# Kernel optimization log

Measured on AMD Instinct MI355X. Metric: run time of the kernel, lower is better.

## Reference

```python
import jax, jax.numpy as jnp
import numpy as np

N_ITER = 3
B, L, U = 32, 120, 640
INPUT_CAPS = 32 * 9 * 12  # 3456
N_CLASSES = 5
FINAL_DIM = 16
N_REL = 25


def squash(x):
    # x: (B, n_caps, dim); squash along dim (axis=2)
    l2 = jnp.sum(x * x, axis=2, keepdims=True)
    return x * (l2 / (1.0 + l2) / jnp.sqrt(l2))


def conv2d(x, w, b, stride):
    out = jax.lax.conv_general_dilated(
        x, w, window_strides=stride, padding='VALID',
        dimension_numbers=('NCHW', 'OIHW', 'NCHW'))
    return out + b[None, :, None, None]


def setup_inputs() -> dict:
    key = jax.random.key(0)
    ks = jax.random.split(key, 10)
    stdv = 1.0 / np.sqrt(INPUT_CAPS)
    return {
        'input': jax.random.normal(ks[0], (B, 1, L, U), jnp.float32),
        'conv1_w': jax.random.normal(ks[1], (256, 1, L // 4, U // 4), jnp.float32) * 0.02,
        'conv1_b': jnp.zeros((256,), jnp.float32),
        'prim_w': jax.random.normal(ks[2], (256, 256, 10, 10), jnp.float32) * 0.02,
        'prim_b': jnp.zeros((256,), jnp.float32),
        'caps_w': jax.random.uniform(ks[3], (INPUT_CAPS, 8, N_CLASSES * FINAL_DIM),
                                     jnp.float32, -stdv, stdv),
        'b_route': jnp.zeros((INPUT_CAPS, N_CLASSES), jnp.float32),
        'pred_w': jax.random.normal(ks[4], (N_REL, FINAL_DIM), jnp.float32) * 0.1,
        'pred_b': jnp.zeros((N_REL,), jnp.float32),
        'eos_w': jax.random.normal(ks[5], (1, FINAL_DIM), jnp.float32) * 0.1,
        'eos_b': jnp.zeros((1,), jnp.float32),
    }


def reference(input, conv1_w, conv1_b, prim_w, prim_b, caps_w, b_route,
              pred_w, pred_b, eos_w, eos_b):
    # conv1 + relu: (B,1,120,640) -> (B,256,91,121)
    x = jax.nn.relu(conv2d(input, conv1_w, conv1_b, (1, 4)))
    # primary caps conv: -> (B,256,9,12)
    out = conv2d(x, prim_w, prim_b, (10, 10))
    n, _, h, w = out.shape
    out = out.reshape(n, 32, 8, h, w)                 # (B,32,8,9,12)
    out = jnp.transpose(out, (0, 1, 3, 4, 2))         # (B,32,9,12,8)
    u = squash(out.reshape(n, -1, 8))                 # (B,3456,8)
    # caps layer prediction: (B,I,8) x (I,8,O*D) -> (B,I,O,D)
    u_predict = jnp.einsum('bic,icj->bij', u, caps_w)
    u_predict = u_predict.reshape(n, INPUT_CAPS, N_CLASSES, FINAL_DIM)
    # agreement routing
    c = jax.nn.softmax(b_route, axis=1)               # (I,O)
    s = jnp.einsum('io,biod->bod', c, u_predict)
    v = squash(s)
    b_batch = jnp.broadcast_to(b_route, (n, INPUT_CAPS, N_CLASSES))
    for _ in range(N_ITER):
        b_batch = b_batch + jnp.einsum('biod,bod->bio', u_predict, v)
        c = jax.nn.softmax(b_batch, axis=-1)          # (B,I,O)
        s = jnp.einsum('bio,biod->bod', c, u_predict)
        v = squash(s)                                 # (B,O,D)
    predict_logits = v @ pred_w.T + pred_b            # (B,O,25)
    eos_logits = v @ eos_w.T + eos_b                  # (B,O,1)
    logits = jnp.concatenate([predict_logits, eos_logits], axis=-1)
    return jax.nn.log_softmax(logits, axis=-1)
```

## Files before the change

kernel.cpp:

```cpp
#include <hip/hip_runtime.h>

typedef __bf16 bf16x8 __attribute__((ext_vector_type(8)));
typedef __bf16 bf16x4 __attribute__((ext_vector_type(4)));
typedef float  f32x4  __attribute__((ext_vector_type(4)));
typedef unsigned int  uint;
typedef unsigned short ushort_t;

static __device__ __forceinline__ ushort_t f2bf(float f) {
    uint u = __float_as_uint(f);
    return (ushort_t)((u + 0x7fffu + ((u >> 16) & 1u)) >> 16);
}
static __device__ __forceinline__ float bf2f(ushort_t u) {
    return __uint_as_float((uint)u << 16);
}
static __device__ __forceinline__ f32x4 up4(uint2 p) {
    f32x4 r;
    r[0] = __uint_as_float(p.x << 16);
    r[1] = __uint_as_float(p.x & 0xffff0000u);
    r[2] = __uint_as_float(p.y << 16);
    r[3] = __uint_as_float(p.y & 0xffff0000u);
    return r;
}


constexpr size_t OFF_W1F = 0;
constexpr size_t SZ_W1F  = (size_t)256 * 4800 * 2;
constexpr size_t OFF_A2  = OFF_W1F + SZ_W1F;
constexpr size_t SZ_A2   = (size_t)256 * 25600 * 2;
constexpr size_t OFF_X   = OFF_A2 + SZ_A2;
constexpr size_t SZ_X    = (size_t)32 * 90 * 120 * 256 * 2;
constexpr size_t OFF_P   = OFF_X + SZ_X;
constexpr size_t SZ_P    = (size_t)8 * 256 * 32 * 112 * 2;
constexpr size_t OFF_UP  = OFF_X;
constexpr size_t OFF_BB  = OFF_X + (size_t)24 * 1024 * 1024;
constexpr size_t OFF_S0  = OFF_X + (size_t)28 * 1024 * 1024;
constexpr size_t OFF_S1  = OFF_X + (size_t)29 * 1024 * 1024;
constexpr size_t WS_NEED = OFF_P + SZ_P;

__global__ void k0_w1(const float* __restrict__ w, ushort_t* __restrict__ o) {
    int t = blockIdx.x * 256 + threadIdx.x;
    int l   = t & 63;
    int q   = t >> 6;
    int kwc = q % 5;
    int ocb = (q / 5) % 16;
    int kh  = q / 80;
    const float* src = w + (size_t)(ocb * 16 + (l & 15)) * 4800 + kh * 160 + kwc * 32 + (l >> 4) * 8;
    float4 f0 = *(const float4*)src;
    float4 f1 = *(const float4*)(src + 4);
    uint4 pk;
    pk.x = (uint)f2bf(f0.x) | ((uint)f2bf(f0.y) << 16);
    pk.y = (uint)f2bf(f0.z) | ((uint)f2bf(f0.w) << 16);
    pk.z = (uint)f2bf(f1.x) | ((uint)f2bf(f1.y) << 16);
    pk.w = (uint)f2bf(f1.z) | ((uint)f2bf(f1.w) << 16);
    *(uint4*)&o[(size_t)t * 8] = pk;
}

__global__ void k0_a2(const float* __restrict__ w, ushort_t* __restrict__ o) {
    __shared__ ushort_t l[25600];
    int oc2 = blockIdx.x;
    const float* src = w + (size_t)oc2 * 25600;
    for (int idx = threadIdx.x; idx < 25600; idx += 256) l[idx] = f2bf(src[idx]);
    __syncthreads();
    ushort_t* dst = o + (size_t)oc2 * 25600;
    for (int idx = threadIdx.x; idx < 25600; idx += 256) {
        int p = idx >> 8, ic = idx & 255;
        dst[idx] = l[ic * 100 + p];
    }
}

__global__ __launch_bounds__(256, 2) void k1_conv1(const float* __restrict__ inp,
                                                   const ushort_t* __restrict__ w1f,
                                                   const float* __restrict__ cb,
                                                   ushort_t* __restrict__ X) {
    __shared__ ushort_t smem[31680];
    ushort_t* brow = smem;
    const int tid = threadIdx.x, lane = tid & 63, wid = tid >> 6;
    const int wm = wid * 64;
    const int h = blockIdx.x, b = blockIdx.y;
    const int l16 = lane & 15, g8 = (lane >> 4) * 8;
    const int bbase = 4 * l16 + g8;
    f32x4 acc[4][8] = {};

    for (int idx = tid; idx < 5280; idx += 256) {
        int r = idx / 176, c = idx % 176;
        uint2 pk; pk.x = 0u; pk.y = 0u;
        if (c < 160) {
            const float* irow = inp + ((size_t)b * 120 + h + r) * 640;
            float4 f = *(const float4*)&irow[c * 4];
            pk.x = (uint)f2bf(f.x) | ((uint)f2bf(f.y) << 16);
            pk.y = (uint)f2bf(f.z) | ((uint)f2bf(f.w) << 16);
        }
        *(uint2*)&brow[r * 704 + c * 4] = pk;
    }
    __syncthreads();

#pragma unroll 1
    for (int kh = 0; kh < 30; ++kh) {
        bf16x8 bc[19];
        const int rb = kh * 704 + bbase;
#pragma unroll
        for (int t = 0; t < 19; ++t) {
            union { bf16x8 v8; bf16x4 v4[2]; } fr;
            fr.v4[0] = *(const bf16x4*)&brow[rb + 32 * t];
            fr.v4[1] = *(const bf16x4*)&brow[rb + 32 * t + 4];
            bc[t] = fr.v8;
        }
#pragma unroll
        for (int kwc = 0; kwc < 5; ++kwc) {
            bf16x8 af[4];
#pragma unroll
            for (int mt = 0; mt < 4; ++mt) {
                int q = (kh * 16 + wid * 4 + mt) * 5 + kwc;
                af[mt] = *(const bf16x8*)&w1f[(size_t)q * 512 + lane * 8];
            }
#pragma unroll
            for (int nt = 0; nt < 8; ++nt)
#pragma unroll
                for (int mt = 0; mt < 4; ++mt)
                    acc[mt][nt] = __builtin_amdgcn_mfma_f32_16x16x32_bf16(af[mt], bc[2 * nt + kwc], acc[mt][nt], 0, 0, 0);
        }
    }

    float cbv[4][4];
#pragma unroll
    for (int mt = 0; mt < 4; ++mt)
#pragma unroll
        for (int r = 0; r < 4; ++r)
            cbv[mt][r] = cb[wm + mt * 16 + (lane >> 4) * 4 + r];
    __syncthreads();
    ushort_t* cs = smem;
#pragma unroll
    for (int nt = 0; nt < 8; ++nt) {
        int wg = nt * 16 + l16;
        if (wg < 120) {
#pragma unroll
            for (int mt = 0; mt < 4; ++mt)
#pragma unroll
                for (int r = 0; r < 4; ++r) {
                    int oc = wm + mt * 16 + (lane >> 4) * 4 + r;
                    float v = acc[mt][nt][r] + cbv[mt][r];
                    v = v > 0.f ? v : 0.f;
                    cs[wg * 264 + oc] = f2bf(v);
                }
        }
    }
    __syncthreads();
    ushort_t* Xbase = X + ((size_t)b * 90 + h) * 120 * 256;
    for (int idx = tid; idx < 3840; idx += 256) {
        int w = idx >> 5, c = (idx & 31) * 8;
        *(uint4*)&Xbase[(size_t)w * 256 + c] = *(const uint4*)&cs[w * 264 + c];
    }
}

__global__ __launch_bounds__(256) void k2_prim(const ushort_t* __restrict__ X,
                                               const ushort_t* __restrict__ A2,
                                               ushort_t* __restrict__ P) {
    const int tid = threadIdx.x, lane = tid & 63, wid = tid >> 6;
    const int mi = blockIdx.x, s = blockIdx.y, b = blockIdx.z;
    const int msub = mi * 128 + wid * 32;
    const int l16 = lane & 15, g8 = (lane >> 4) * 8;
    f32x4 acc[2][7] = {};
    size_t aoff[2];
#pragma unroll
    for (int t = 0; t < 2; ++t) aoff[t] = (size_t)(msub + t * 16 + l16) * 25600 + g8;
    size_t noff[7];
#pragma unroll
    for (int nt = 0; nt < 7; ++nt) {
        int n = nt * 16 + l16; n = n < 108 ? n : 107;
        int h2 = n / 12, w2 = n % 12;
        noff[nt] = (((size_t)b * 90 + 10 * h2) * 120 + 10 * w2) * 256 + g8;
    }
    const int p0 = (100 * s) / 8, p1 = (100 * (s + 1)) / 8;
#pragma unroll 1
    for (int p = p0; p < p1; ++p) {
        int ph = p / 10, pw = p % 10;
        size_t xb = (size_t)(ph * 120 + pw) * 256;
        size_t ab = (size_t)p * 256;
#pragma unroll
        for (int icc = 0; icc < 8; ++icc) {
            bf16x8 af[2], bfr[7];
#pragma unroll
            for (int t = 0; t < 2; ++t)
                af[t] = *(const bf16x8*)&A2[aoff[t] + ab + icc * 32];
#pragma unroll
            for (int nt = 0; nt < 7; ++nt)
                bfr[nt] = *(const bf16x8*)&X[noff[nt] + xb + icc * 32];
#pragma unroll
            for (int t = 0; t < 2; ++t)
#pragma unroll
                for (int nt = 0; nt < 7; ++nt)
                    acc[t][nt] = __builtin_amdgcn_mfma_f32_16x16x32_bf16(af[t], bfr[nt], acc[t][nt], 0, 0, 0);
        }
    }
#pragma unroll
    for (int t = 0; t < 2; ++t)
#pragma unroll
        for (int nt = 0; nt < 7; ++nt)
#pragma unroll
            for (int r = 0; r < 4; ++r) {
                int n   = nt * 16 + l16;
                int oc2 = msub + t * 16 + (lane >> 4) * 4 + r;
                P[(((size_t)s * 256 + oc2) * 32 + b) * 112 + n] = f2bf(acc[t][nt][r]);
            }
}

__global__ __launch_bounds__(256) void k3_caps(const ushort_t* __restrict__ P,
                                               const float* __restrict__ prim_b,
                                               const float* __restrict__ caps_w,
                                               ushort_t* __restrict__ UP) {
    int t = blockIdx.x * 256 + threadIdx.x;
    int b = t & 31, i = t >> 5;
    int cap = i / 108, hw = i % 108;
    float ud[8], l2 = 0.f;
#pragma unroll
    for (int d = 0; d < 8; ++d) {
        int oc2 = cap * 8 + d;
        float v = prim_b[oc2];
#pragma unroll
        for (int s = 0; s < 8; ++s)
            v += bf2f(P[(((size_t)s * 256 + oc2) * 32 + b) * 112 + hw]);
        ud[d] = v; l2 += v * v;
    }
    float scale = sqrtf(l2) / (1.f + l2);
#pragma unroll
    for (int d = 0; d < 8; ++d) ud[d] *= scale;
    const float* cw = caps_w + (size_t)i * 640;
    ushort_t* up = UP + ((size_t)b * 3456 + i) * 80;
    for (int j = 0; j < 80; j += 4) {
        f32x4 o = {0.f, 0.f, 0.f, 0.f};
#pragma unroll
        for (int d = 0; d < 8; ++d) {
            f32x4 w = *(const f32x4*)&cw[d * 80 + j];
            o += ud[d] * w;
        }
        uint2 pk;
        pk.x = (uint)f2bf(o[0]) | ((uint)f2bf(o[1]) << 16);
        pk.y = (uint)f2bf(o[2]) | ((uint)f2bf(o[3]) << 16);
        *(uint2*)&up[j] = pk;
    }
}

__global__ __launch_bounds__(128) void k4_iter(const ushort_t* __restrict__ UP,
                                               const float* __restrict__ b_route,
                                               float* __restrict__ BB,
                                               const float* __restrict__ spIn,
                                               float* __restrict__ spOut,
                                               int flags) {
    __shared__ __attribute__((aligned(16))) float sv[80];
    __shared__ float sred[2][80];
    __shared__ float sscale[5];
    const int tid = threadIdx.x, lane = tid & 63, wv = tid >> 6;
    const int chunk = blockIdx.x, b = blockIdx.y;

    if (flags & 1) {
        if (tid < 80) {
            float s = 0.f;
            for (int c2 = 0; c2 < 27; ++c2) s += spIn[((size_t)b * 27 + c2) * 80 + tid];
            sv[tid] = s;
        }
        __syncthreads();
        if (tid < 5) {
            float l2 = 0.f;
            for (int d = 0; d < 16; ++d) { float x = sv[tid * 16 + d]; l2 += x * x; }
            sscale[tid] = sqrtf(l2) / (1.f + l2);
        }
        __syncthreads();
        if (tid < 80) sv[tid] *= sscale[tid / 16];
    }
    __syncthreads();

    const int i = chunk * 128 + tid;
    const ushort_t* up = UP + ((size_t)b * 3456 + i) * 80;
    f32x4 u4[20];
#pragma unroll
    for (int r = 0; r < 20; ++r) u4[r] = up4(*(const uint2*)&up[r * 4]);

    float bo[5];
#pragma unroll
    for (int o = 0; o < 5; ++o) {
        float bv = (flags & 2) ? BB[((size_t)b * 3456 + i) * 5 + o] : b_route[i * 5 + o];
        if (flags & 1) {
            f32x4 dv = u4[o * 4 + 0] * (*(const f32x4*)&sv[o * 16 + 0])
                     + u4[o * 4 + 1] * (*(const f32x4*)&sv[o * 16 + 4])
                     + u4[o * 4 + 2] * (*(const f32x4*)&sv[o * 16 + 8])
                     + u4[o * 4 + 3] * (*(const f32x4*)&sv[o * 16 + 12]);
            bv += dv[0] + dv[1] + dv[2] + dv[3];
        }
        if (flags & 4) BB[((size_t)b * 3456 + i) * 5 + o] = bv;
        bo[o] = bv;
    }
    float m = fmaxf(fmaxf(fmaxf(bo[0], bo[1]), fmaxf(bo[2], bo[3])), bo[4]);
    float e[5], sum = 0.f;
#pragma unroll
    for (int o = 0; o < 5; ++o) { e[o] = __expf(bo[o] - m); sum += e[o]; }
    float inv = 1.f / sum;
    f32x4 a4[20];
#pragma unroll
    for (int o = 0; o < 5; ++o) {
        float c = e[o] * inv;
#pragma unroll
        for (int q = 0; q < 4; ++q) a4[o * 4 + q] = c * u4[o * 4 + q];
    }
#pragma unroll
    for (int off = 32; off >= 1; off >>= 1)
#pragma unroll
        for (int q = 0; q < 20; ++q)
#pragma unroll
            for (int c = 0; c < 4; ++c) a4[q][c] += __shfl_xor(a4[q][c], off, 64);
    if (lane == 0)
#pragma unroll
        for (int q = 0; q < 20; ++q)
#pragma unroll
            for (int c = 0; c < 4; ++c) sred[wv][q * 4 + c] = a4[q][c];
    __syncthreads();
    if (tid < 80) spOut[((size_t)b * 27 + chunk) * 80 + tid] = sred[0][tid] + sred[1][tid];
}

__global__ __launch_bounds__(192) void k4_fin(const float* __restrict__ spIn,
                                              const float* __restrict__ pred_w,
                                              const float* __restrict__ pred_b,
                                              const float* __restrict__ eos_w,
                                              const float* __restrict__ eos_b,
                                              float* __restrict__ out) {
    __shared__ __attribute__((aligned(16))) float sv[80];
    __shared__ float sscale[5];
    __shared__ float lg[130];
    __shared__ float lse[5];
    const int tid = threadIdx.x, b = blockIdx.x;
    if (tid < 80) {
        float s = 0.f;
        for (int c2 = 0; c2 < 27; ++c2) s += spIn[((size_t)b * 27 + c2) * 80 + tid];
        sv[tid] = s;
    }
    __syncthreads();
    if (tid < 5) {
        float l2 = 0.f;
        for (int d = 0; d < 16; ++d) { float x = sv[tid * 16 + d]; l2 += x * x; }
        sscale[tid] = sqrtf(l2) / (1.f + l2);
    }
    __syncthreads();
    if (tid < 80) sv[tid] *= sscale[tid / 16];
    __syncthreads();
    if (tid < 130) {
        int o = tid / 26, j = tid % 26;
        const float* wv = (j < 25) ? &pred_w[j * 16] : &eos_w[0];
        float dot = (j < 25) ? pred_b[j] : eos_b[0];
        for (int d = 0; d < 16; ++d) dot += sv[o * 16 + d] * wv[d];
        lg[tid] = dot;
    }
    __syncthreads();
    if (tid < 5) {
        float m = lg[tid * 26];
        for (int j = 1; j < 26; ++j) m = fmaxf(m, lg[tid * 26 + j]);
        float sum = 0.f;
        for (int j = 0; j < 26; ++j) sum += expf(lg[tid * 26 + j] - m);
        lse[tid] = m + logf(sum);
    }
    __syncthreads();
    if (tid < 130) out[b * 130 + tid] = lg[tid] - lse[tid / 26];
}

extern "C" void kernel_launch(void* const* d_in, const int* in_sizes, int n_in,
                              void* d_out, int out_size, void* d_ws, size_t ws_size,
                              hipStream_t stream) {
    const float* inp    = (const float*)d_in[0];
    const float* w1     = (const float*)d_in[1];
    const float* cb1    = (const float*)d_in[2];
    const float* w2     = (const float*)d_in[3];
    const float* pb2    = (const float*)d_in[4];
    const float* capsw  = (const float*)d_in[5];
    const float* broute = (const float*)d_in[6];
    const float* predw  = (const float*)d_in[7];
    const float* predb  = (const float*)d_in[8];
    const float* eosw   = (const float*)d_in[9];
    const float* eosb   = (const float*)d_in[10];
    float* out = (float*)d_out;
    char* ws = (char*)d_ws;
    if (ws_size < WS_NEED) return;

    ushort_t* w1f = (ushort_t*)(ws + OFF_W1F);
    ushort_t* a2  = (ushort_t*)(ws + OFF_A2);
    ushort_t* X   = (ushort_t*)(ws + OFF_X);
    ushort_t* P   = (ushort_t*)(ws + OFF_P);
    ushort_t* UP  = (ushort_t*)(ws + OFF_UP);
    float*    BB  = (float*)(ws + OFF_BB);
    float*    S0  = (float*)(ws + OFF_S0);
    float*    S1  = (float*)(ws + OFF_S1);

    k0_w1   <<<dim3(600),      dim3(256), 0, stream>>>(w1, w1f);
    k0_a2   <<<dim3(256),      dim3(256), 0, stream>>>(w2, a2);
    k1_conv1<<<dim3(90, 32),   dim3(256), 0, stream>>>(inp, w1f, cb1, X);
    k2_prim <<<dim3(2, 8, 32), dim3(256), 0, stream>>>(X, a2, P);
    k3_caps <<<dim3(432),      dim3(256), 0, stream>>>(P, pb2, capsw, UP);
    k4_iter <<<dim3(27, 32),   dim3(128), 0, stream>>>(UP, broute, BB, S1, S0, 0);
    k4_iter <<<dim3(27, 32),   dim3(128), 0, stream>>>(UP, broute, BB, S0, S1, 1 | 4);
    k4_iter <<<dim3(27, 32),   dim3(128), 0, stream>>>(UP, broute, BB, S1, S0, 1 | 2 | 4);
    k4_iter <<<dim3(27, 32),   dim3(128), 0, stream>>>(UP, broute, BB, S0, S1, 1 | 2);
    k4_fin  <<<dim3(32),       dim3(192), 0, stream>>>(S1, predw, predb, eosw, eosb, out);
}
```

Before: 1.033 ms.

## Fuse weight prep, atomic split-K for prim conv, fold initial routing into caps kernel

Merges the two weight-conversion kernels into one launch. Doubles the split-K factor of the primary-caps conv and accumulates partial sums with fp32 atomics into a zeroed buffer, removing the bf16 partial buffer and the 8-way reduction in the caps kernel. The caps kernel now also computes the initial uniform-softmax weighted sum s0 via shared-memory reduction and atomics, eliminating one routing iteration launch. This adds a zeroing kernel and atomic contention, and makes the float summation order nondeterministic.

Result: no change. 1.049 ms (+1.5%).

```diff
diff --git a/kernel.cpp b/kernel.cpp
--- a/kernel.cpp
+++ b/kernel.cpp
@@ -9,9 +9,6 @@
 static __device__ __forceinline__ ushort_t f2bf(float f) {
     uint u = __float_as_uint(f);
     return (ushort_t)((u + 0x7fffu + ((u >> 16) & 1u)) >> 16);
-}
-static __device__ __forceinline__ float bf2f(ushort_t u) {
-    return __uint_as_float((uint)u << 16);
 }
 static __device__ __forceinline__ f32x4 up4(uint2 p) {
     f32x4 r;
@@ -30,41 +27,50 @@
 constexpr size_t OFF_X   = OFF_A2 + SZ_A2;
 constexpr size_t SZ_X    = (size_t)32 * 90 * 120 * 256 * 2;
 constexpr size_t OFF_P   = OFF_X + SZ_X;
-constexpr size_t SZ_P    = (size_t)8 * 256 * 32 * 112 * 2;
+constexpr size_t SZ_P    = (size_t)256 * 32 * 112 * 4;
+constexpr size_t OFF_S0F = OFF_P + SZ_P;
+constexpr size_t SZ_S0F  = (size_t)32 * 80 * 4;
+constexpr size_t OFF_SC0 = OFF_S0F + SZ_S0F;
+constexpr size_t SZ_SC   = (size_t)32 * 27 * 80 * 4;
+constexpr size_t OFF_SC1 = OFF_SC0 + SZ_SC;
 constexpr size_t OFF_UP  = OFF_X;
 constexpr size_t OFF_BB  = OFF_X + (size_t)24 * 1024 * 1024;
-constexpr size_t OFF_S0  = OFF_X + (size_t)28 * 1024 * 1024;
-constexpr size_t OFF_S1  = OFF_X + (size_t)29 * 1024 * 1024;
-constexpr size_t WS_NEED = OFF_P + SZ_P;
-
-__global__ void k0_w1(const float* __restrict__ w, ushort_t* __restrict__ o) {
-    int t = blockIdx.x * 256 + threadIdx.x;
-    int l   = t & 63;
-    int q   = t >> 6;
-    int kwc = q % 5;
-    int ocb = (q / 5) % 16;
-    int kh  = q / 80;
-    const float* src = w + (size_t)(ocb * 16 + (l & 15)) * 4800 + kh * 160 + kwc * 32 + (l >> 4) * 8;
-    float4 f0 = *(const float4*)src;
-    float4 f1 = *(const float4*)(src + 4);
-    uint4 pk;
-    pk.x = (uint)f2bf(f0.x) | ((uint)f2bf(f0.y) << 16);
-    pk.y = (uint)f2bf(f0.z) | ((uint)f2bf(f0.w) << 16);
-    pk.z = (uint)f2bf(f1.x) | ((uint)f2bf(f1.y) << 16);
-    pk.w = (uint)f2bf(f1.z) | ((uint)f2bf(f1.w) << 16);
-    *(uint4*)&o[(size_t)t * 8] = pk;
-}
-
-__global__ void k0_a2(const float* __restrict__ w, ushort_t* __restrict__ o) {
+constexpr size_t WS_NEED = OFF_SC1 + SZ_SC;
+
+__global__ void k_zero(f32x4* __restrict__ z) {
+    int i = blockIdx.x * 256 + threadIdx.x;
+    if (i < 230016) z[i] = f32x4{0.f, 0.f, 0.f, 0.f};
+}
+
+__global__ void k0_prep(const float* __restrict__ w1, const float* __restrict__ w2,
+                        ushort_t* __restrict__ w1f, ushort_t* __restrict__ a2) {
     __shared__ ushort_t l[25600];
-    int oc2 = blockIdx.x;
-    const float* src = w + (size_t)oc2 * 25600;
-    for (int idx = threadIdx.x; idx < 25600; idx += 256) l[idx] = f2bf(src[idx]);
-    __syncthreads();
-    ushort_t* dst = o + (size_t)oc2 * 25600;
-    for (int idx = threadIdx.x; idx < 25600; idx += 256) {
-        int p = idx >> 8, ic = idx & 255;
-        dst[idx] = l[ic * 100 + p];
+    if (blockIdx.x < 600) {
+        int t = blockIdx.x * 256 + threadIdx.x;
+        int ln  = t & 63;
+        int q   = t >> 6;
+        int kwc = q % 5;
+        int ocb = (q / 5) % 16;
+        int kh  = q / 80;
+        const float* src = w1 + (size_t)(ocb * 16 + (ln & 15)) * 4800 + kh * 160 + kwc * 32 + (ln >> 4) * 8;
+        float4 f0 = *(const float4*)src;
+        float4 f1 = *(const float4*)(src + 4);
+        uint4 pk;
+        pk.x = (uint)f2bf(f0.x) | ((uint)f2bf(f0.y) << 16);
+        pk.y = (uint)f2bf(f0.z) | ((uint)f2bf(f0.w) << 16);
+        pk.z = (uint)f2bf(f1.x) | ((uint)f2bf(f1.y) << 16);
+        pk.w = (uint)f2bf(f1.z) | ((uint)f2bf(f1.w) << 16);
+        *(uint4*)&w1f[(size_t)t * 8] = pk;
+    } else {
+        int oc2 = blockIdx.x - 600;
+        const float* src = w2 + (size_t)oc2 * 25600;
+        for (int idx = threadIdx.x; idx < 25600; idx += 256) l[idx] = f2bf(src[idx]);
+        __syncthreads();
+        ushort_t* dst = a2 + (size_t)oc2 * 25600;
+        for (int idx = threadIdx.x; idx < 25600; idx += 256) {
+            int p = idx >> 8, ic = idx & 255;
+            dst[idx] = l[ic * 100 + p];
+        }
     }
 }
 
@@ -154,7 +160,7 @@
 
 __global__ __launch_bounds__(256) void k2_prim(const ushort_t* __restrict__ X,
                                                const ushort_t* __restrict__ A2,
-                                               ushort_t* __restrict__ P) {
+                                               float* __restrict__ P) {
     const int tid = threadIdx.x, lane = tid & 63, wid = tid >> 6;
     const int mi = blockIdx.x, s = blockIdx.y, b = blockIdx.z;
     const int msub = mi * 128 + wid * 32;
@@ -170,7 +176,7 @@
         int h2 = n / 12, w2 = n % 12;
         noff[nt] = (((size_t)b * 90 + 10 * h2) * 120 + 10 * w2) * 256 + g8;
     }
-    const int p0 = (100 * s) / 8, p1 = (100 * (s + 1)) / 8;
+    const int p0 = (100 * s) / 16, p1 = (100 * (s + 1)) / 16;
 #pragma unroll 1
     for (int p = p0; p < p1; ++p) {
         int ph = p / 10, pw = p % 10;
@@ -200,30 +206,43 @@
             for (int r = 0; r < 4; ++r) {
                 int n   = nt * 16 + l16;
                 int oc2 = msub + t * 16 + (lane >> 4) * 4 + r;
-                P[(((size_t)s * 256 + oc2) * 32 + b) * 112 + n] = f2bf(acc[t][nt][r]);
+                unsafeAtomicAdd(&P[((size_t)oc2 * 32 + b) * 112 + n], acc[t][nt][r]);
             }
 }
 
-__global__ __launch_bounds__(256) void k3_caps(const ushort_t* __restrict__ P,
+__global__ __launch_bounds__(256) void k3_caps(const float* __restrict__ P,
                                                const float* __restrict__ prim_b,
                                                const float* __restrict__ caps_w,
-                                               ushort_t* __restrict__ UP) {
+                                               const float* __restrict__ b_route,
+                                               ushort_t* __restrict__ UP,
+                                               float* __restrict__ S0F) {
+    __shared__ float sred[4][32][81];
     int t = blockIdx.x * 256 + threadIdx.x;
     int b = t & 31, i = t >> 5;
+    const int lane = threadIdx.x & 63, wv = threadIdx.x >> 6;
     int cap = i / 108, hw = i % 108;
     float ud[8], l2 = 0.f;
 #pragma unroll
     for (int d = 0; d < 8; ++d) {
         int oc2 = cap * 8 + d;
-        float v = prim_b[oc2];
-#pragma unroll
-        for (int s = 0; s < 8; ++s)
-            v += bf2f(P[(((size_t)s * 256 + oc2) * 32 + b) * 112 + hw]);
+        float v = prim_b[oc2] + P[((size_t)oc2 * 32 + b) * 112 + hw];
         ud[d] = v; l2 += v * v;
     }
     float scale = sqrtf(l2) / (1.f + l2);
 #pragma unroll
     for (int d = 0; d < 8; ++d) ud[d] *= scale;
+    const float* br = b_route + (size_t)i * 5;
+    float bo[5];
+#pragma unroll
+    for (int o = 0; o < 5; ++o) bo[o] = br[o];
+    float m = fmaxf(fmaxf(fmaxf(bo[0], bo[1]), fmaxf(bo[2], bo[3])), bo[4]);
+    float e[5], es = 0.f;
+#pragma unroll
+    for (int o = 0; o < 5; ++o) { e[o] = __expf(bo[o] - m); es += e[o]; }
+    float inv = 1.f / es;
+#pragma unroll
+    for (int o = 0; o < 5; ++o) e[o] *= inv;
+
     const float* cw = caps_w + (size_t)i * 640;
     ushort_t* up = UP + ((size_t)b * 3456 + i) * 80;
     for (int j = 0; j < 80; j += 4) {
@@ -237,6 +256,19 @@
         pk.x = (uint)f2bf(o[0]) | ((uint)f2bf(o[1]) << 16);
         pk.y = (uint)f2bf(o[2]) | ((uint)f2bf(o[3]) << 16);
         *(uint2*)&up[j] = pk;
+        f32x4 con = e[j >> 4] * o;
+#pragma unroll
+        for (int c = 0; c < 4; ++c) con[c] += __shfl_xor(con[c], 32, 64);
+        if (lane < 32) {
+            float* sr = &sred[wv][lane][j];
+            sr[0] = con[0]; sr[1] = con[1]; sr[2] = con[2]; sr[3] = con[3];
+        }
+    }
+    __syncthreads();
+    for (int k = threadIdx.x; k < 2560; k += 256) {
+        int bb = k / 80, j = k % 80;
+        float s = sred[0][bb][j] + sred[1][bb][j] + sred[2][bb][j] + sred[3][bb][j];
+        unsafeAtomicAdd(&S0F[bb * 80 + j], s);
     }
 }
 
@@ -254,8 +286,12 @@
 
     if (flags & 1) {
         if (tid < 80) {
-            float s = 0.f;
-            for (int c2 = 0; c2 < 27; ++c2) s += spIn[((size_t)b * 27 + c2) * 80 + tid];
+            float s;
+            if (flags & 8) s = spIn[(size_t)b * 80 + tid];
+            else {
+                s = 0.f;
+                for (int c2 = 0; c2 < 27; ++c2) s += spIn[((size_t)b * 27 + c2) * 80 + tid];
+            }
             sv[tid] = s;
         }
         __syncthreads();
@@ -279,13 +315,11 @@
 #pragma unroll
     for (int o = 0; o < 5; ++o) {
         float bv = (flags & 2) ? BB[((size_t)b * 3456 + i) * 5 + o] : b_route[i * 5 + o];
-        if (flags & 1) {
-            f32x4 dv = u4[o * 4 + 0] * (*(const f32x4*)&sv[o * 16 + 0])
-                     + u4[o * 4 + 1] * (*(const f32x4*)&sv[o * 16 + 4])
-                     + u4[o * 4 + 2] * (*(const f32x4*)&sv[o * 16 + 8])
-                     + u4[o * 4 + 3] * (*(const f32x4*)&sv[o * 16 + 12]);
-            bv += dv[0] + dv[1] + dv[2] + dv[3];
-        }
+        f32x4 dv = u4[o * 4 + 0] * (*(const f32x4*)&sv[o * 16 + 0])
+                 + u4[o * 4 + 1] * (*(const f32x4*)&sv[o * 16 + 4])
+                 + u4[o * 4 + 2] * (*(const f32x4*)&sv[o * 16 + 8])
+                 + u4[o * 4 + 3] * (*(const f32x4*)&sv[o * 16 + 12]);
+        bv += dv[0] + dv[1] + dv[2] + dv[3];
         if (flags & 4) BB[((size_t)b * 3456 + i) * 5 + o] = bv;
         bo[o] = bv;
     }
@@ -381,20 +415,20 @@
     ushort_t* w1f = (ushort_t*)(ws + OFF_W1F);
     ushort_t* a2  = (ushort_t*)(ws + OFF_A2);
     ushort_t* X   = (ushort_t*)(ws + OFF_X);
-    ushort_t* P   = (ushort_t*)(ws + OFF_P);
+    float*    P   = (float*)(ws + OFF_P);
+    float*    S0F = (float*)(ws + OFF_S0F);
+    float*    SC0 = (float*)(ws + OFF_SC0);
+    float*    SC1 = (float*)(ws + OFF_SC1);
     ushort_t* UP  = (ushort_t*)(ws + OFF_UP);
     float*    BB  = (float*)(ws + OFF_BB);
-    float*    S0  = (float*)(ws + OFF_S0);
-    float*    S1  = (float*)(ws + OFF_S1);
-
-    k0_w1   <<<dim3(600),      dim3(256), 0, stream>>>(w1, w1f);
-    k0_a2   <<<dim3(256),      dim3(256), 0, stream>>>(w2, a2);
-    k1_conv1<<<dim3(90, 32),   dim3(256), 0, stream>>>(inp, w1f, cb1, X);
-    k2_prim <<<dim3(2, 8, 32), dim3(256), 0, stream>>>(X, a2, P);
-    k3_caps <<<dim3(432),      dim3(256), 0, stream>>>(P, pb2, capsw, UP);
-    k4_iter <<<dim3(27, 32),   dim3(128), 0, stream>>>(UP, broute, BB, S1, S0, 0);
-    k4_iter <<<dim3(27, 32),   dim3(128), 0, stream>>>(UP, broute, BB, S0, S1, 1 | 4);
-    k4_iter <<<dim3(27, 32),   dim3(128), 0, stream>>>(UP, broute, BB, S1, S0, 1 | 2 | 4);
-    k4_iter <<<dim3(27, 32),   dim3(128), 0, stream>>>(UP, broute, BB, S0, S1, 1 | 2);
-    k4_fin  <<<dim3(32),       dim3(192), 0, stream>>>(S1, predw, predb, eosw, eosb, out);
-}
+
+    k_zero  <<<dim3(899),       dim3(256), 0, stream>>>((f32x4*)P);
+    k0_prep <<<dim3(856),       dim3(256), 0, stream>>>(w1, w2, w1f, a2);
+    k1_conv1<<<dim3(90, 32),    dim3(256), 0, stream>>>(inp, w1f, cb1, X);
+    k2_prim <<<dim3(2, 16, 32), dim3(256), 0, stream>>>(X, a2, P);
+    k3_caps <<<dim3(432),       dim3(256), 0, stream>>>(P, pb2, capsw, broute, UP, S0F);
+    k4_iter <<<dim3(27, 32),    dim3(128), 0, stream>>>(UP, broute, BB, S0F, SC1, 1 | 4 | 8);
+    k4_iter <<<dim3(27, 32),    dim3(128), 0, stream>>>(UP, broute, BB, SC1, SC0, 1 | 2 | 4);
+    k4_iter <<<dim3(27, 32),    dim3(128), 0, stream>>>(UP, broute, BB, SC0, SC1, 1 | 2);
+    k4_fin  <<<dim3(32),        dim3(192), 0, stream>>>(SC1, predw, predb, eosw, eosb, out);
+}
```
